# Performance work log

Hardware: AMD Instinct MI355X
Metric: run time of the kernel (lower is better)

Reference implementation:

```python
import jax, jax.numpy as jnp
import numpy as np

B, T, HS, WS = 4, 16, 32, 64          # batch, time, lat, lon
D_MODEL, N_HEADS = 256, 8
E = D_MODEL // N_HEADS                 # 32 per-head dim
MODES = [8, 8, 16]
F_LAST = WS // 2 + 1                   # 33 rfft bins on last dim
M_LAST = MODES[-1]                     # 16 kept rfft bins
M_PANEL = MODES[0] * MODES[1]          # 64 kept (T,HS) panel modes


def _sym_indexes(shape):
    # faithful numpy port of get_symmetry_index_in_fft_pannel
    shape = np.array(shape)
    idx = np.stack([t.flatten() for t in np.meshgrid(*[range(s) for s in shape])])
    idx2 = (-idx) % shape[:, None]
    fftshift = (idx + shape[:, None] // 2) % shape[:, None]
    center = (shape[:, None] - 1) / 2
    order = np.argsort(np.linalg.norm(fftshift - center, axis=0))
    idx = idx[:, order]
    idx2 = idx2[:, order]
    return np.ravel_multi_index(idx, shape), np.ravel_multi_index(idx2, shape)


def _picked_panel():
    # lowest-frequency mode selection honoring Hermitian pairing
    i1, i2 = _sym_indexes((T, HS))
    picked = []
    for a, b in zip(i1, i2):
        if a in picked or b in picked:
            continue
        picked.append(a)
        if len(picked) == M_PANEL:
            break
    return np.array(picked, dtype=np.int32), i1.astype(np.int32), i2.astype(np.int32)


def setup_inputs() -> dict:
    key = jax.random.key(0)
    ks = jax.random.split(key, 12)
    sl = 1.0 / np.float32(np.sqrt(D_MODEL))
    sw = np.float32(0.02)
    panel, s1, s2 = _picked_panel()
    return {
        "x": jax.random.normal(ks[0], (B, T, HS, WS, D_MODEL), jnp.float32),
        "Wq": jax.random.normal(ks[1], (D_MODEL, D_MODEL), jnp.float32) * sl,
        "bq": jnp.zeros((D_MODEL,), jnp.float32),
        "Wk": jax.random.normal(ks[2], (D_MODEL, D_MODEL), jnp.float32) * sl,
        "bk": jnp.zeros((D_MODEL,), jnp.float32),
        "Wv": jax.random.normal(ks[3], (D_MODEL, D_MODEL), jnp.float32) * sl,
        "bv": jnp.zeros((D_MODEL,), jnp.float32),
        "Wo": jax.random.normal(ks[4], (D_MODEL, D_MODEL), jnp.float32) * sl,
        "bo": jnp.zeros((D_MODEL,), jnp.float32),
        "w_real": jax.random.normal(ks[5], (N_HEADS, E, E, M_PANEL, M_LAST), jnp.float32) * sw,
        "w_imag": jax.random.normal(ks[6], (N_HEADS, E, E, M_PANEL, M_LAST), jnp.float32) * sw,
        "panel_idx": jnp.asarray(panel),
        "sym_idx1": jnp.asarray(s1),
        "sym_idx2": jnp.asarray(s2),
    }


def reference(x, Wq, bq, Wk, bk, Wv, bv, Wo, bo, w_real, w_imag,
              panel_idx, sym_idx1, sym_idx2):
    # QKV projections (the torch layer computes all three; FourierBlockN uses q)
    q = (x @ Wq + bq).reshape(B, T, HS, WS, N_HEADS, E).transpose(0, 4, 5, 1, 2, 3)
    _k = (x @ Wk + bk)
    _v = (x @ Wv + bv)
    # rfftn over the spacetime dims -> (B,H,E,T,HS,F_LAST)
    x_ft = jnp.fft.rfftn(q, axes=(-3, -2, -1)).reshape(B, N_HEADS, E, T * HS, F_LAST)
    # gather selected frequency modes
    x_sel = x_ft[:, :, :, panel_idx, :M_LAST]                    # (B,H,E,Mp,Ml)
    w = w_real + 1j * w_imag                                      # (H,E,E,Mp,Ml)
    out_sel = jnp.einsum('bhipf,hiopf->bhopf', x_sel, w)
    out_ft = jnp.zeros_like(x_ft)
    out_ft = out_ft.at[:, :, :, panel_idx, :M_LAST].set(out_sel)
    # canonical_fft_freq: enforce Hermitian symmetry on the (T,HS) panel
    out_ft = out_ft.at[:, :, :, sym_idx1, :].set(
        (out_ft[:, :, :, sym_idx1, :] + jnp.conj(out_ft[:, :, :, sym_idx2, :])) * 0.5)
    out_ft = out_ft.reshape(B, N_HEADS, E, T, HS, F_LAST)
    o = jnp.fft.irfftn(out_ft, s=(T, HS, WS), axes=(-3, -2, -1))  # (B,H,E,T,HS,WS)
    o = o.transpose(0, 3, 4, 5, 1, 2).reshape(B, T, HS, WS, N_HEADS * E)
    return o @ Wo + bo
```

## Files before the change

### kernel.cpp

```cpp
#include <hip/hip_runtime.h>
#include <hip/hip_bf16.h>
#include <cmath>

#define BB 4
#define TT 16
#define HH 32
#define WW 64
#define DD 256
#define NHEAD 8
#define EE 32
#define MP 64
#define ML 16
#define SPAT 32768
#define S2D 512

constexpr size_t OFF_FTRE = 0;
constexpr size_t OFF_FTIM = 1024;
constexpr size_t OFF_FHRE = 2048;
constexpr size_t OFF_FHIM = 4096;
constexpr size_t OFF_CW   = 6144;
constexpr size_t OFF_W64I = 7168;
constexpr size_t OFF_W16  = 9216;
constexpr size_t OFF_FHT  = 9728;
constexpr size_t OFF_GB   = 16384;
constexpr size_t OFF_FW   = OFF_GB + 8388608;
constexpr size_t OFF_X    = OFF_FW + 16777216;
constexpr size_t OFF_V    = OFF_X + 2097152;
constexpr size_t OFF_WT   = OFF_V + 2097152;

typedef short short8 __attribute__((ext_vector_type(8)));
typedef float f32x4 __attribute__((ext_vector_type(4)));

static __device__ __forceinline__ unsigned short f2bf(float x) {
  union { float f; unsigned u; } v; v.f = x;
  unsigned r = v.u + 0x7fffu + ((v.u >> 16) & 1u);
  return (unsigned short)(r >> 16);
}

static __device__ __forceinline__ void gl_lds16(const void* g, void* l) {
  __builtin_amdgcn_global_load_lds((const __attribute__((address_space(1))) void*)g,
                                   (__attribute__((address_space(3))) void*)l, 16, 0, 0);
}

static __device__ __forceinline__ void xcd_tile_dg(int flat, int& tile, int& dg) {
  int w8 = flat >> 3, xl = flat & 7;
  tile = ((w8 >> 2) << 3) | xl;
  dg = w8 & 3;
}

static __device__ __forceinline__ void xcd_tile_dg2(int flat, int& tile, int& dg) {
  int w8 = flat >> 3, xl = flat & 7;
  tile = ((w8 >> 1) << 3) | xl;
  dg = w8 & 1;
}

__global__ __launch_bounds__(256) void k0_tables(const int* __restrict__ panel, float* __restrict__ tab) {
  __shared__ int kt[MP], kh[MP];
  int tid = threadIdx.x;
  if (tid < MP) { int s = panel[tid]; kt[tid] = s >> 5; kh[tid] = s & 31; }
  __syncthreads();
  const double PI2 = 6.283185307179586476925286766559;
  for (int i = tid; i < 1024; i += 256) {
    int p = i >> 4, t = i & 15;
    double a = -PI2 * (double)((t * kt[p]) & 15) / 16.0;
    tab[OFF_FTRE + i] = (float)cos(a);
    tab[OFF_FTIM + i] = (float)sin(a);
  }
  for (int i = tid; i < 2048; i += 256) {
    int p = i >> 5, hs = i & 31;
    double a = -PI2 * (double)((hs * kh[p]) & 31) / 32.0;
    tab[OFF_FHRE + i] = (float)cos(a);
    tab[OFF_FHIM + i] = (float)sin(a);
  }
  for (int i = tid; i < 1024; i += 256) {
    int f = i >> 6, wsx = i & 63;
    double a = PI2 * (double)((f * wsx) & 63) / 64.0;
    tab[OFF_CW + i] = (f == 0) ? (1.0f / 64.0f) : (float)(2.0 * cos(a) / 64.0);
  }
  for (int i = tid; i < 2048; i += 256) {
    int wsx = i >> 5, f2 = i & 31; int f = f2 >> 1;
    double a = -PI2 * (double)((wsx * f) & 63) / 64.0;
    tab[OFF_W64I + i] = (f2 & 1) ? (float)sin(a) : (float)cos(a);
  }
  if (tid < 256) {
    int t = tid >> 4, k = tid & 15;
    double a = -PI2 * (double)((t * k) & 15) / 16.0;
    tab[OFF_W16 + 2 * tid]     = (float)cos(a);
    tab[OFF_W16 + 2 * tid + 1] = (float)sin(a);
  }
  for (int i = tid; i < 2048; i += 256) {
    int hs = i >> 6, p = i & 63;
    double a = -PI2 * (double)((hs * kh[p]) & 31) / 32.0;
    tab[OFF_FHT + 2 * i]     = (float)cos(a);
    tab[OFF_FHT + 2 * i + 1] = (float)sin(a);
  }
}

__global__ __launch_bounds__(256) void conv_w(const float* __restrict__ Wq, const float* __restrict__ Wo,
                                              unsigned short* __restrict__ wqt, unsigned short* __restrict__ wot) {
  __shared__ float tile[32][33];
  const float* src = blockIdx.z ? Wo : Wq;
  unsigned short* dst = blockIdx.z ? wot : wqt;
  int k0 = blockIdx.x * 32, d0 = blockIdx.y * 32;
  int tx = threadIdx.x & 31, r4 = threadIdx.x >> 5;
  #pragma unroll
  for (int it = 0; it < 4; it++) {
    int row = r4 + it * 8;
    tile[row][tx] = src[(size_t)(k0 + row) * 256 + d0 + tx];
  }
  __syncthreads();
  #pragma unroll
  for (int it = 0; it < 4; it++) {
    int row = r4 + it * 8;
    dst[(size_t)(d0 + row) * 256 + k0 + tx] = f2bf(tile[tx][row]);
  }
}

__global__ __launch_bounds__(512) void k1f4(const float* __restrict__ x,
                                            const unsigned short* __restrict__ wqt,
                                            const float* __restrict__ bq,
                                            const float* __restrict__ tabp,
                                            float* __restrict__ Fwg) {
  __shared__ char smem[75776];
  char*  Al = smem;
  char*  Bl = smem + 16384;
  float* QL = (float*)smem;
  float* WL = (float*)(smem + 67584);
  int tile, dg;
  xcd_tile_dg2(blockIdx.x, tile, dg);
  int d0 = dg << 7;
  int b = tile >> 8, st = tile & 255;
  int sp0 = st << 7;
  int tid = threadIdx.x;
  int lane = tid & 63, w = tid >> 6;
  int l15 = lane & 15, kg = lane >> 4;
  int swz = (l15 & 7) << 4;
  for (int i = tid; i < 2048; i += 512) WL[i] = tabp[OFF_W64I + i];
  f32x4 acc[8];
  #pragma unroll
  for (int ni = 0; ni < 8; ni++) acc[ni] = (f32x4){0.f, 0.f, 0.f, 0.f};
  const float* xbase = x + ((size_t)b * 32768 + sp0) * 256;
  const char* Bbase = (const char*)(wqt + (size_t)d0 * 256);
  for (int k0 = 0; k0 < 256; k0 += 64) {
    #pragma unroll
    for (int it = 0; it < 2; it++) {
      int o = it * 8192 + tid * 16;
      int row = o >> 7, cb = o & 127;
      gl_lds16(Bbase + (size_t)row * 512 + k0 * 2 + (cb ^ ((row & 7) << 4)), Bl + o);
    }
    #pragma unroll
    for (int it = 0; it < 2; it++) {
      int idx = it * 512 + tid;
      int row = idx >> 3, g8 = idx & 7;
      const float* src = xbase + (size_t)row * 256 + k0 + g8 * 8;
      float4 a4 = *reinterpret_cast<const float4*>(src);
      float4 b4 = *reinterpret_cast<const float4*>(src + 4);
      short8 v;
      v[0] = (short)f2bf(a4.x); v[1] = (short)f2bf(a4.y); v[2] = (short)f2bf(a4.z); v[3] = (short)f2bf(a4.w);
      v[4] = (short)f2bf(b4.x); v[5] = (short)f2bf(b4.y); v[6] = (short)f2bf(b4.z); v[7] = (short)f2bf(b4.w);
      int byteoff = (row * 128 + g8 * 16) ^ ((row & 7) << 4);
      *reinterpret_cast<short8*>(Al + byteoff) = v;
    }
    __syncthreads();
    #pragma unroll
    for (int ks = 0; ks < 2; ks++) {
      int koff = (ks * 64 + kg * 16) ^ swz;
      short8 af = *reinterpret_cast<const short8*>(Al + (w * 16 + l15) * 128 + koff);
      #pragma unroll
      for (int ni = 0; ni < 8; ni++) {
        short8 bfr = *reinterpret_cast<const short8*>(Bl + (ni * 16 + l15) * 128 + koff);
        acc[ni] = __builtin_amdgcn_mfma_f32_16x16x32_bf16(af, bfr, acc[ni], 0, 0, 0);
      }
    }
    __syncthreads();
  }
  #pragma unroll
  for (int ni = 0; ni < 8; ni++) {
    float bqv = bq[d0 + ni * 16 + l15];
    f32x4 vv = acc[ni];
    int m = w * 16 + kg * 4;
    #pragma unroll
    for (int j = 0; j < 4; j++)
      QL[(m + j) * 132 + ni * 16 + l15] = vv[j] + bqv;
  }
  __syncthreads();
  {
    int sg = tid >> 8, rem = tid & 255;
    int dp = rem >> 3, f2q = rem & 7;
    f32x4 a2[4];
    a2[0] = (f32x4){0.f, 0.f, 0.f, 0.f};
    a2[1] = (f32x4){0.f, 0.f, 0.f, 0.f};
    a2[2] = (f32x4){0.f, 0.f, 0.f, 0.f};
    a2[3] = (f32x4){0.f, 0.f, 0.f, 0.f};
    const float* qbase = QL + (sg * 64) * 132 + dp * 4;
    const float* wbase = WL + f2q * 4;
    #pragma unroll 8
    for (int wsx = 0; wsx < 64; wsx++) {
      f32x4 q  = *reinterpret_cast<const f32x4*>(qbase + wsx * 132);
      f32x4 wv = *reinterpret_cast<const f32x4*>(wbase + wsx * 32);
      a2[0] += wv * q[0];
      a2[1] += wv * q[1];
      a2[2] += wv * q[2];
      a2[3] += wv * q[3];
    }
    int sgl = st * 2 + sg;
    size_t g0 = ((size_t)(b * 512 + sgl) * 256 + d0 + dp * 4) * 32 + f2q * 4;
    #pragma unroll
    for (int di = 0; di < 4; di++)
      *reinterpret_cast<f32x4*>(&Fwg[g0 + (size_t)di * 32]) = a2[di];
  }
}

__global__ __launch_bounds__(512) void k3f(const float* __restrict__ Fwg, const float* __restrict__ tabp,
                                           const int* __restrict__ panel, float* __restrict__ X) {
  __shared__ float2 Floc[8192];
  __shared__ float2 fhT[32][64];
  __shared__ float2 W16L[16][16];
  __shared__ int ktl[64];
  int bd = blockIdx.x; int b = bd >> 8; int d = bd & 255;
  int tid = threadIdx.x;
  if (tid < 256) W16L[tid >> 4][tid & 15] = reinterpret_cast<const float2*>(tabp + OFF_W16)[tid];
  for (int i = tid; i < 2048; i += 512) fhT[i >> 6][i & 63] = reinterpret_cast<const float2*>(tabp + OFF_FHT)[i];
  if (tid < 64) ktl[tid] = panel[tid] >> 5;
  {
    const char* gb = (const char*)Fwg;
    #pragma unroll
    for (int r = 0; r < 8; r++) {
      int o = r * 8192 + tid * 16;
      int s = o >> 7; int c16 = (o >> 4) & 7;
      size_t gaddr = ((size_t)(b * 512 + s) * 256 + d) * 128 + (size_t)c16 * 16;
      gl_lds16(gb + gaddr, (char*)Floc + o);
    }
  }
  __syncthreads();
  int hs = tid >> 4, f = tid & 15;
  float2 v[16];
  #pragma unroll
  for (int t = 0; t < 16; t++) v[t] = Floc[(t * 32 + hs) * 16 + f];
  float2 a[16];
  #pragma unroll
  for (int k = 0; k < 16; k++) a[k] = make_float2(0.f, 0.f);
  #pragma unroll
  for (int t = 0; t < 16; t++) {
    float2 vv = v[t];
    #pragma unroll
    for (int k = 0; k < 16; k++) {
      float2 w = W16L[t][k];
      a[k].x += w.x * vv.x - w.y * vv.y;
      a[k].y += w.x * vv.y + w.y * vv.x;
    }
  }
  #pragma unroll
  for (int k = 0; k < 16; k++) Floc[(k * 32 + hs) * 16 + f] = a[k];
  __syncthreads();
  int p2 = tid >> 4;
  float2 res[2];
  #pragma unroll
  for (int half = 0; half < 2; half++) {
    int p = p2 + half * 32;
    int kt = ktl[p];
    float ar = 0.f, ai = 0.f;
    #pragma unroll 8
    for (int h = 0; h < 32; h++) {
      float2 e = fhT[h][p];
      float2 u = Floc[(kt * 32 + h) * 16 + f];
      ar += u.x * e.x - u.y * e.y;
      ai += u.x * e.y + u.y * e.x;
    }
    res[half] = make_float2(ar, ai);
  }
  float2* Xo = reinterpret_cast<float2*>(X) + (size_t)bd * 1024;
  Xo[p2 * 16 + f] = res[0];
  Xo[(p2 + 32) * 16 + f] = res[1];
}

__global__ __launch_bounds__(512) void k3b_mix(const float* __restrict__ X, const float* __restrict__ wreal,
                                               const float* __restrict__ wimag, float* __restrict__ V) {
  __shared__ float2 xs[4][32][16];
  int h = blockIdx.x >> 6;
  int p = blockIdx.x & 63;
  int tid = threadIdx.x;
  const float2* Xv = reinterpret_cast<const float2*>(X);
  for (int i = tid; i < 2048; i += 512) {
    int b = i >> 9, ii = (i >> 4) & 31, f = i & 15;
    xs[b][ii][f] = Xv[((size_t)(b * 256 + h * 32 + ii) * MP + p) * ML + f];
  }
  __syncthreads();
  int o = tid >> 4, f = tid & 15;
  float accr[4] = {0, 0, 0, 0}, acci[4] = {0, 0, 0, 0};
  for (int i = 0; i < 32; i++) {
    size_t wofs = ((((size_t)h * 32 + i) * 32 + o) * MP + p) * ML + f;
    float wr = wreal[wofs], wi = wimag[wofs];
    #pragma unroll
    for (int b = 0; b < 4; b++) {
      float2 xv = xs[b][i][f];
      accr[b] += xv.x * wr - xv.y * wi;
      acci[b] += xv.x * wi + xv.y * wr;
    }
  }
  #pragma unroll
  for (int b = 0; b < 4; b++)
    reinterpret_cast<float2*>(V)[((size_t)(b * 256 + h * 32 + o) * MP + p) * ML + f] =
        make_float2(accr[b], acci[b]);
}

__global__ __launch_bounds__(256) void k4a_inv(const float* __restrict__ V, const float* __restrict__ tabp,
                                               float* __restrict__ gbuf) {
  __shared__ float2 vl[64][16];
  __shared__ float2 ft[64][16];
  __shared__ float2 fh[64][32];
  int bd = blockIdx.x;
  int tid = threadIdx.x;
  const float2* Vv = reinterpret_cast<const float2*>(V) + (size_t)bd * MP * ML;
  for (int i = tid; i < 1024; i += 256) {
    vl[i >> 4][i & 15] = Vv[i];
    ft[i >> 4][i & 15] = make_float2(tabp[OFF_FTRE + i], tabp[OFF_FTIM + i]);
  }
  for (int i = tid; i < 2048; i += 256) fh[i >> 5][i & 31] = make_float2(tabp[OFF_FHRE + i], tabp[OFF_FHIM + i]);
  __syncthreads();
  float g0[16], g1[16];
  #pragma unroll
  for (int f = 0; f < 16; f++) { g0[f] = 0.f; g1[f] = 0.f; }
  int s0 = tid * 2;
  int t0 = s0 >> 5, hs0 = s0 & 31;
  int t1 = (s0 + 1) >> 5, hs1 = (s0 + 1) & 31;
  for (int p = 0; p < 64; p++) {
    float2 et0 = ft[p][t0], eh0 = fh[p][hs0];
    float2 et1 = ft[p][t1], eh1 = fh[p][hs1];
    float er0 = et0.x * eh0.x - et0.y * eh0.y;
    float ei0 = et0.x * eh0.y + et0.y * eh0.x;
    float er1 = et1.x * eh1.x - et1.y * eh1.y;
    float ei1 = et1.x * eh1.y + et1.y * eh1.x;
    #pragma unroll
    for (int f = 0; f < 16; f++) {
      float2 v = vl[p][f];
      g0[f] += v.x * er0 + v.y * ei0;
      g1[f] += v.x * er1 + v.y * ei1;
    }
  }
  float4* gb = reinterpret_cast<float4*>(gbuf + (size_t)bd * 8192 + (size_t)s0 * 16);
  #pragma unroll
  for (int q = 0; q < 4; q++)
    gb[q] = make_float4(g0[q * 4] * (1.f / 512.f), g0[q * 4 + 1] * (1.f / 512.f),
                        g0[q * 4 + 2] * (1.f / 512.f), g0[q * 4 + 3] * (1.f / 512.f));
  #pragma unroll
  for (int q = 0; q < 4; q++)
    gb[4 + q] = make_float4(g1[q * 4] * (1.f / 512.f), g1[q * 4 + 1] * (1.f / 512.f),
                            g1[q * 4 + 2] * (1.f / 512.f), g1[q * 4 + 3] * (1.f / 512.f));
}

__global__ __launch_bounds__(256) void k4b_cos(const float* __restrict__ gbuf, const float* __restrict__ tabp,
                                               unsigned short* __restrict__ ob) {
  __shared__ float Gs[256][17];
  __shared__ float cwL[16][64];
  int s = blockIdx.x, b = blockIdx.y;
  int tid = threadIdx.x;
  for (int i = tid; i < 4096; i += 256) {
    int c = i >> 4, f = i & 15;
    Gs[c][f] = gbuf[(size_t)(b * 256 + c) * 8192 + s * 16 + f];
  }
  for (int i = tid; i < 1024; i += 256) cwL[i >> 6][i & 63] = tabp[OFF_CW + i];
  __syncthreads();
  int c0 = (tid & 63) * 4, wsg = tid >> 6;
  float gv[4][16];
  #pragma unroll
  for (int j = 0; j < 4; j++)
    #pragma unroll
    for (int f = 0; f < 16; f++) gv[j][f] = Gs[c0 + j][f];
  for (int wsi = 0; wsi < 16; wsi++) {
    int wsx = wsg * 16 + wsi;
    float a0 = 0.f, a1 = 0.f, a2 = 0.f, a3 = 0.f;
    #pragma unroll
    for (int f = 0; f < 16; f++) {
      float cwv = cwL[f][wsx];
      a0 += gv[0][f] * cwv; a1 += gv[1][f] * cwv; a2 += gv[2][f] * cwv; a3 += gv[3][f] * cwv;
    }
    ushort4 u;
    u.x = f2bf(a0); u.y = f2bf(a1); u.z = f2bf(a2); u.w = f2bf(a3);
    *reinterpret_cast<ushort4*>(&ob[((size_t)b * SPAT + (size_t)s * 64 + wsx) * 256 + c0]) = u;
  }
}

__global__ __launch_bounds__(256) void k5_mfma(const unsigned short* __restrict__ ob,
                                               const unsigned short* __restrict__ wot,
                                               const float* __restrict__ bo, float* __restrict__ out) {
  __shared__ char smem[34816];
  unsigned short* Al = (unsigned short*)smem;
  unsigned short* Bl = (unsigned short*)(smem + 16384);
  float* OL = (float*)smem;
  int tile, dg;
  xcd_tile_dg(blockIdx.x, tile, dg);
  int b = tile >> 8, sp0 = (tile & 255) << 7, d0 = dg << 6;
  int tid = threadIdx.x;
  int lane = tid & 63, w = tid >> 6;
  int l15 = lane & 15, kg = lane >> 4;
  int swz = (l15 & 7) << 4;
  f32x4 acc[2][4];
  #pragma unroll
  for (int mi = 0; mi < 2; mi++)
    #pragma unroll
    for (int ni = 0; ni < 4; ni++) acc[mi][ni] = (f32x4){0.f, 0.f, 0.f, 0.f};
  const char* Abase = (const char*)(ob + ((size_t)b * 32768 + sp0) * 256);
  const char* Bbase = (const char*)(wot + (size_t)d0 * 256);
  for (int k0 = 0; k0 < 256; k0 += 64) {
    #pragma unroll
    for (int it = 0; it < 2; it++) {
      int o = tid * 16 + it * 4096 + 16384;
      int ol = o - 16384;
      int row = ol >> 7, cb = ol & 127;
      int scb = cb ^ ((row & 7) << 4);
      gl_lds16(Bbase + (size_t)row * 512 + k0 * 2 + scb, smem + o);
    }
    #pragma unroll
    for (int it = 0; it < 4; it++) {
      int o = tid * 16 + it * 4096;
      int row = o >> 7, cb = o & 127;
      int scb = cb ^ ((row & 7) << 4);
      gl_lds16(Abase + (size_t)row * 512 + k0 * 2 + scb, (char*)Al + o);
    }
    __syncthreads();
    #pragma unroll
    for (int ks = 0; ks < 2; ks++) {
      int koff = (ks * 64 + kg * 16) ^ swz;
      short8 af[2], bfr[4];
      #pragma unroll
      for (int mi = 0; mi < 2; mi++)
        af[mi] = *(const short8*)((const char*)Al + (w * 32 + mi * 16 + l15) * 128 + koff);
      #pragma unroll
      for (int ni = 0; ni < 4; ni++)
        bfr[ni] = *(const short8*)((const char*)Bl + (ni * 16 + l15) * 128 + koff);
      #pragma unroll
      for (int mi = 0; mi < 2; mi++)
        #pragma unroll
        for (int ni = 0; ni < 4; ni++)
          acc[mi][ni] = __builtin_amdgcn_mfma_f32_16x16x32_bf16(af[mi], bfr[ni], acc[mi][ni], 0, 0, 0);
    }
    __syncthreads();
  }
  #pragma unroll
  for (int ni = 0; ni < 4; ni++) {
    float bov = bo[d0 + ni * 16 + l15];
    #pragma unroll
    for (int mi = 0; mi < 2; mi++) {
      f32x4 v = acc[mi][ni];
      int m = w * 32 + mi * 16 + kg * 4;
      #pragma unroll
      for (int j = 0; j < 4; j++)
        OL[(m + j) * 68 + ni * 16 + l15] = v[j] + bov;
    }
  }
  __syncthreads();
  int f4 = tid & 15, r0 = tid >> 4;
  #pragma unroll
  for (int r = 0; r < 8; r++) {
    int m = r * 16 + r0;
    float4 val = *reinterpret_cast<const float4*>(&OL[m * 68 + f4 * 4]);
    *reinterpret_cast<float4*>(&out[((size_t)b * SPAT + sp0 + m) * 256 + d0 + f4 * 4]) = val;
  }
}

extern "C" void kernel_launch(void* const* d_in, const int* in_sizes, int n_in,
                              void* d_out, int out_size, void* d_ws, size_t ws_size,
                              hipStream_t stream) {
  const float* x  = (const float*)d_in[0];
  const float* Wq = (const float*)d_in[1];
  const float* bq = (const float*)d_in[2];
  const float* Wo = (const float*)d_in[7];
  const float* bo = (const float*)d_in[8];
  const float* wr = (const float*)d_in[9];
  const float* wi = (const float*)d_in[10];
  const int* panel = (const int*)d_in[11];
  float* wsf = (float*)d_ws;
  float* out = (float*)d_out;

  float*          gbuf = wsf + OFF_GB;
  unsigned short* obb  = (unsigned short*)(wsf + OFF_FW);
  unsigned short* wqt  = (unsigned short*)(wsf + OFF_WT);
  unsigned short* wot  = wqt + 65536;

  k0_tables<<<dim3(1), dim3(256), 0, stream>>>(panel, wsf);
  conv_w<<<dim3(8, 8, 2), dim3(256), 0, stream>>>(Wq, Wo, wqt, wot);
  k1f4<<<dim3(2048), dim3(512), 0, stream>>>(x, wqt, bq, wsf, wsf + OFF_FW);
  k3f<<<dim3(1024), dim3(512), 0, stream>>>(wsf + OFF_FW, wsf, panel, wsf + OFF_X);
  k3b_mix<<<dim3(512), dim3(512), 0, stream>>>(wsf + OFF_X, wr, wi, wsf + OFF_V);
  k4a_inv<<<dim3(1024), dim3(256), 0, stream>>>(wsf + OFF_V, wsf, gbuf);
  k4b_cos<<<dim3(512, 4), dim3(256), 0, stream>>>(gbuf, wsf, obb);
  k5_mfma<<<dim3(4096), dim3(256), 0, stream>>>(obb, wot, bo, out);
}
```

Baseline: 320.6 us.

## Fuse inverse cosine transform into output projection GEMM via LDS

Merges the k4b_cos kernel, which builds the bf16 spatial activations along the last axis, into the Wo projection MFMA kernel. The activation tile for one spatial row is now computed straight into swizzled LDS and fed to MFMA without ever being written to and read back from a global bf16 buffer. Each block covers 64 rows and all 256 output channels, reloading 32-column Wo slices per iteration. The cost is large LDS use (about 70KB), which lowers occupancy, and more barriers per block, with only one B buffer per loop step.

New measurement: 303.7 us (median of 2 runs). 1.06x faster.

```diff
diff --git a/kernel.cpp b/kernel.cpp
--- a/kernel.cpp
+++ b/kernel.cpp
@@ -349,113 +349,110 @@
                             g1[q * 4 + 2] * (1.f / 512.f), g1[q * 4 + 3] * (1.f / 512.f));
 }
 
-__global__ __launch_bounds__(256) void k4b_cos(const float* __restrict__ gbuf, const float* __restrict__ tabp,
-                                               unsigned short* __restrict__ ob) {
-  __shared__ float Gs[256][17];
-  __shared__ float cwL[16][64];
-  int s = blockIdx.x, b = blockIdx.y;
-  int tid = threadIdx.x;
+__global__ __launch_bounds__(256) void k5f2(const float* __restrict__ gbuf,
+                                            const unsigned short* __restrict__ wot,
+                                            const float* __restrict__ bo,
+                                            const float* __restrict__ tabp,
+                                            float* __restrict__ out) {
+  __shared__ char smem[70656];
+  float* Gs  = (float*)smem;
+  float* cwL = (float*)(smem + 17408);
+  char*  Asm = smem + 21504;
+  char*  Bl  = smem + 54272;
+  float* OL  = (float*)smem;
+  int tile, sh;
+  xcd_tile_dg2(blockIdx.x, tile, sh);
+  int b = tile >> 8, spair = tile & 255;
+  int s = spair * 2 + sh;
+  int tid = threadIdx.x;
+  int lane = tid & 63, w = tid >> 6;
+  int l15 = lane & 15, kg = lane >> 4;
   for (int i = tid; i < 4096; i += 256) {
     int c = i >> 4, f = i & 15;
-    Gs[c][f] = gbuf[(size_t)(b * 256 + c) * 8192 + s * 16 + f];
-  }
-  for (int i = tid; i < 1024; i += 256) cwL[i >> 6][i & 63] = tabp[OFF_CW + i];
-  __syncthreads();
-  int c0 = (tid & 63) * 4, wsg = tid >> 6;
-  float gv[4][16];
-  #pragma unroll
-  for (int j = 0; j < 4; j++)
-    #pragma unroll
-    for (int f = 0; f < 16; f++) gv[j][f] = Gs[c0 + j][f];
-  for (int wsi = 0; wsi < 16; wsi++) {
-    int wsx = wsg * 16 + wsi;
-    float a0 = 0.f, a1 = 0.f, a2 = 0.f, a3 = 0.f;
-    #pragma unroll
-    for (int f = 0; f < 16; f++) {
-      float cwv = cwL[f][wsx];
-      a0 += gv[0][f] * cwv; a1 += gv[1][f] * cwv; a2 += gv[2][f] * cwv; a3 += gv[3][f] * cwv;
-    }
-    ushort4 u;
-    u.x = f2bf(a0); u.y = f2bf(a1); u.z = f2bf(a2); u.w = f2bf(a3);
-    *reinterpret_cast<ushort4*>(&ob[((size_t)b * SPAT + (size_t)s * 64 + wsx) * 256 + c0]) = u;
-  }
-}
-
-__global__ __launch_bounds__(256) void k5_mfma(const unsigned short* __restrict__ ob,
-                                               const unsigned short* __restrict__ wot,
-                                               const float* __restrict__ bo, float* __restrict__ out) {
-  __shared__ char smem[34816];
-  unsigned short* Al = (unsigned short*)smem;
-  unsigned short* Bl = (unsigned short*)(smem + 16384);
-  float* OL = (float*)smem;
-  int tile, dg;
-  xcd_tile_dg(blockIdx.x, tile, dg);
-  int b = tile >> 8, sp0 = (tile & 255) << 7, d0 = dg << 6;
-  int tid = threadIdx.x;
-  int lane = tid & 63, w = tid >> 6;
-  int l15 = lane & 15, kg = lane >> 4;
-  int swz = (l15 & 7) << 4;
-  f32x4 acc[2][4];
-  #pragma unroll
-  for (int mi = 0; mi < 2; mi++)
-    #pragma unroll
-    for (int ni = 0; ni < 4; ni++) acc[mi][ni] = (f32x4){0.f, 0.f, 0.f, 0.f};
-  const char* Abase = (const char*)(ob + ((size_t)b * 32768 + sp0) * 256);
-  const char* Bbase = (const char*)(wot + (size_t)d0 * 256);
-  for (int k0 = 0; k0 < 256; k0 += 64) {
-    #pragma unroll
-    for (int it = 0; it < 2; it++) {
-      int o = tid * 16 + it * 4096 + 16384;
-      int ol = o - 16384;
-      int row = ol >> 7, cb = ol & 127;
-      int scb = cb ^ ((row & 7) << 4);
-      gl_lds16(Bbase + (size_t)row * 512 + k0 * 2 + scb, smem + o);
-    }
+    Gs[c * 17 + f] = gbuf[(size_t)(b * 256 + c) * 8192 + s * 16 + f];
+  }
+  for (int i = tid; i < 1024; i += 256) cwL[i] = tabp[OFF_CW + i];
+  __syncthreads();
+  {
+    int c0 = (tid & 63) * 4, wsg = tid >> 6;
+    float gv[4][16];
+    #pragma unroll
+    for (int j = 0; j < 4; j++)
+      #pragma unroll
+      for (int f = 0; f < 16; f++) gv[j][f] = Gs[(c0 + j) * 17 + f];
+    for (int wsi = 0; wsi < 16; wsi++) {
+      int wsx = wsg * 16 + wsi;
+      float a0 = 0.f, a1 = 0.f, a2 = 0.f, a3 = 0.f;
+      #pragma unroll
+      for (int f = 0; f < 16; f++) {
+        float cwv = cwL[f * 64 + wsx];
+        a0 += gv[0][f] * cwv; a1 += gv[1][f] * cwv; a2 += gv[2][f] * cwv; a3 += gv[3][f] * cwv;
+      }
+      ushort4 u;
+      u.x = f2bf(a0); u.y = f2bf(a1); u.z = f2bf(a2); u.w = f2bf(a3);
+      int kbyte = c0 * 2;
+      int kc = kbyte >> 7, rem = kbyte & 127;
+      int addr = kc * 8192 + wsx * 128 + (rem ^ ((wsx & 7) << 4));
+      *reinterpret_cast<ushort4*>(Asm + addr) = u;
+    }
+  }
+  const char* Bbase = (const char*)wot;
+  {
     #pragma unroll
     for (int it = 0; it < 4; it++) {
-      int o = tid * 16 + it * 4096;
-      int row = o >> 7, cb = o & 127;
-      int scb = cb ^ ((row & 7) << 4);
-      gl_lds16(Abase + (size_t)row * 512 + k0 * 2 + scb, (char*)Al + o);
+      int chunk = it * 4 + w;
+      int kc = chunk & 3, dgrp = chunk >> 2;
+      int d = dgrp * 8 + (lane >> 3);
+      int kbs = kc * 128 + (((lane & 7) << 4) ^ ((d & 7) << 4));
+      gl_lds16(Bbase + (size_t)d * 512 + kbs, Bl + kc * 4096 + dgrp * 1024 + lane * 16);
+    }
+  }
+  __syncthreads();
+  float* outb = out + ((size_t)b * 32768 + (size_t)s * 64) * 256;
+  for (int it8 = 0; it8 < 8; it8++) {
+    int d0g = it8 * 32;
+    f32x4 acc0 = (f32x4){0.f, 0.f, 0.f, 0.f};
+    f32x4 acc1 = (f32x4){0.f, 0.f, 0.f, 0.f};
+    #pragma unroll
+    for (int step = 0; step < 8; step++) {
+      int kc = step >> 1;
+      int rembase = (step & 1) * 64 + kg * 16;
+      int arow = w * 16 + l15;
+      short8 af  = *reinterpret_cast<const short8*>(Asm + kc * 8192 + arow * 128 + (rembase ^ ((arow & 7) << 4)));
+      short8 bf0 = *reinterpret_cast<const short8*>(Bl + kc * 4096 + l15 * 128 + (rembase ^ ((l15 & 7) << 4)));
+      short8 bf1 = *reinterpret_cast<const short8*>(Bl + kc * 4096 + (16 + l15) * 128 + (rembase ^ (((16 + l15) & 7) << 4)));
+      acc0 = __builtin_amdgcn_mfma_f32_16x16x32_bf16(af, bf0, acc0, 0, 0, 0);
+      acc1 = __builtin_amdgcn_mfma_f32_16x16x32_bf16(af, bf1, acc1, 0, 0, 0);
+    }
+    {
+      float bo0 = bo[d0g + l15];
+      float bo1 = bo[d0g + 16 + l15];
+      #pragma unroll
+      for (int j = 0; j < 4; j++) {
+        OL[(w * 16 + kg * 4 + j) * 36 + l15]      = acc0[j] + bo0;
+        OL[(w * 16 + kg * 4 + j) * 36 + 16 + l15] = acc1[j] + bo1;
+      }
     }
     __syncthreads();
-    #pragma unroll
-    for (int ks = 0; ks < 2; ks++) {
-      int koff = (ks * 64 + kg * 16) ^ swz;
-      short8 af[2], bfr[4];
+    if (it8 < 7) {
+      int dnext = (it8 + 1) * 32;
       #pragma unroll
-      for (int mi = 0; mi < 2; mi++)
-        af[mi] = *(const short8*)((const char*)Al + (w * 32 + mi * 16 + l15) * 128 + koff);
-      #pragma unroll
-      for (int ni = 0; ni < 4; ni++)
-        bfr[ni] = *(const short8*)((const char*)Bl + (ni * 16 + l15) * 128 + koff);
-      #pragma unroll
-      for (int mi = 0; mi < 2; mi++)
-        #pragma unroll
-        for (int ni = 0; ni < 4; ni++)
-          acc[mi][ni] = __builtin_amdgcn_mfma_f32_16x16x32_bf16(af[mi], bfr[ni], acc[mi][ni], 0, 0, 0);
+      for (int it = 0; it < 4; it++) {
+        int chunk = it * 4 + w;
+        int kc = chunk & 3, dgrp = chunk >> 2;
+        int d = dgrp * 8 + (lane >> 3);
+        int kbs = kc * 128 + (((lane & 7) << 4) ^ ((d & 7) << 4));
+        gl_lds16(Bbase + (size_t)(dnext + d) * 512 + kbs, Bl + kc * 4096 + dgrp * 1024 + lane * 16);
+      }
+    }
+    #pragma unroll
+    for (int rep = 0; rep < 2; rep++) {
+      int row = (tid >> 3) + rep * 32;
+      int f4 = tid & 7;
+      float4 v = *reinterpret_cast<const float4*>(OL + row * 36 + f4 * 4);
+      *reinterpret_cast<float4*>(outb + (size_t)row * 256 + d0g + f4 * 4) = v;
     }
     __syncthreads();
-  }
-  #pragma unroll
-  for (int ni = 0; ni < 4; ni++) {
-    float bov = bo[d0 + ni * 16 + l15];
-    #pragma unroll
-    for (int mi = 0; mi < 2; mi++) {
-      f32x4 v = acc[mi][ni];
-      int m = w * 32 + mi * 16 + kg * 4;
-      #pragma unroll
-      for (int j = 0; j < 4; j++)
-        OL[(m + j) * 68 + ni * 16 + l15] = v[j] + bov;
-    }
-  }
-  __syncthreads();
-  int f4 = tid & 15, r0 = tid >> 4;
-  #pragma unroll
-  for (int r = 0; r < 8; r++) {
-    int m = r * 16 + r0;
-    float4 val = *reinterpret_cast<const float4*>(&OL[m * 68 + f4 * 4]);
-    *reinterpret_cast<float4*>(&out[((size_t)b * SPAT + sp0 + m) * 256 + d0 + f4 * 4]) = val;
   }
 }
 
@@ -474,7 +471,6 @@
   float* out = (float*)d_out;
 
   float*          gbuf = wsf + OFF_GB;
-  unsigned short* obb  = (unsigned short*)(wsf + OFF_FW);
   unsigned short* wqt  = (unsigned short*)(wsf + OFF_WT);
   unsigned short* wot  = wqt + 65536;
 
@@ -484,6 +480,5 @@
   k3f<<<dim3(1024), dim3(512), 0, stream>>>(wsf + OFF_FW, wsf, panel, wsf + OFF_X);
   k3b_mix<<<dim3(512), dim3(512), 0, stream>>>(wsf + OFF_X, wr, wi, wsf + OFF_V);
   k4a_inv<<<dim3(1024), dim3(256), 0, stream>>>(wsf + OFF_V, wsf, gbuf);
-  k4b_cos<<<dim3(512, 4), dim3(256), 0, stream>>>(gbuf, wsf, obb);
-  k5_mfma<<<dim3(4096), dim3(256), 0, stream>>>(obb, wot, bo, out);
-}
+  k5f2<<<dim3(2048), dim3(256), 0, stream>>>(gbuf, wot, bo, wsf, out);
+}
```
